# Kernel optimization log

Measured on AMD Instinct MI355X. Metric: run time of the kernel, lower is better.

The kernel has to match this reference:

```python
import jax, jax.numpy as jnp
import numpy as np

B, S, D = 4, 1024, 1024
L, H, DK, DV, DFF = 2, 8, 128, 128, 2048
MASK_VALUE = -1e-30
LN_EPS = 1e-14  # K.epsilon()**2 with K.epsilon()=1e-7


def _glorot(key, shape):
    fan_in, fan_out = shape[-2], shape[-1]
    lim = np.sqrt(6.0 / (fan_in + fan_out)).astype(np.float32)
    return jax.random.uniform(key, shape, jnp.float32, -lim, lim)


def setup_inputs() -> dict:
    key = jax.random.key(0)
    ks = jax.random.split(key, 8)
    return {
        "x": jax.random.normal(ks[0], (B, S, D), jnp.float32),
        "mask": jnp.ones((B, S), jnp.float32),
        "Wq": _glorot(ks[1], (L, H, D, DK)),
        "Wk": _glorot(ks[2], (L, H, D, DK)),
        "Wv": _glorot(ks[3], (L, H, D, DV)),
        "Wo": _glorot(ks[4], (L, H * DV, D)),
        "W1": _glorot(ks[5], (L, D, DFF)),
        "b1": jnp.zeros((L, DFF), jnp.float32),
        "W2": _glorot(ks[6], (L, DFF, D)),
        "b2": jnp.zeros((L, D), jnp.float32),
        "gamma": jnp.ones((2 * L,), jnp.float32),
        "beta": jnp.zeros((2 * L,), jnp.float32),
    }


def _layernorm(x, g, b):
    mean = jnp.mean(x, axis=-1, keepdims=True)
    var = jnp.mean(jnp.square(x - mean), axis=-1, keepdims=True)
    return (x - mean) / jnp.sqrt(var + LN_EPS) * g + b


def reference(x, mask, Wq, Wk, Wv, Wo, W1, b1, W2, b2, gamma, beta):
    m = mask[:, None, None, :]  # [B,1,1,S] broadcast over heads and query positions
    num_layers = Wq.shape[0]
    for i in range(num_layers):
        # All heads at once (faithful to the per-head loop: identical math)
        q = jnp.einsum("bsd,hdk->bhsk", x, Wq[i])
        k = jnp.einsum("bsd,hdk->bhsk", x, Wk[i])
        v = jnp.einsum("bsd,hdv->bhsv", x, Wv[i])
        A = jnp.einsum("bhsk,bhtk->bhst", q, k)  # NOTE: no 1/sqrt(dk) scaling in original
        A = m * A + (1.0 - m) * MASK_VALUE
        A = jax.nn.softmax(A, axis=-1)
        o = jnp.einsum("bhst,bhtv->bhsv", A, v)
        conc = o.transpose(0, 2, 1, 3).reshape(x.shape[0], x.shape[1], -1)  # [B,S,H*DV]
        proj = conc @ Wo[i]
        x = _layernorm(x + proj, gamma[2 * i], beta[2 * i])
        ffn = jax.nn.relu(x @ W1[i] + b1[i]) @ W2[i] + b2[i]
        x = _layernorm(x + ffn, gamma[2 * i + 1], beta[2 * i + 1])
    return x
```

## Files before the change

kernel.cpp:

```cpp
#include <hip/hip_runtime.h>
#include <hip/hip_bf16.h>


typedef __bf16 bf16_t;
typedef bf16_t bf16x8 __attribute__((ext_vector_type(8)));
typedef bf16_t bf16x4v __attribute__((ext_vector_type(4)));
typedef float f32x4 __attribute__((ext_vector_type(4)));

#define MFMA16(a, b, c) __builtin_amdgcn_mfma_f32_16x16x32_bf16((a), (b), (c), 0, 0, 0)

__device__ __align__(256) unsigned char g_ws[(size_t)192 << 20];

#define MBOFF(x) ((size_t)(x) << 20)
#define OFF_X32 MBOFF(0)
#define OFF_XB_HI MBOFF(16)
#define OFF_XB_LO MBOFF(24)
#define OFF_QKV_HI MBOFF(32)
#define OFF_QKV_LO MBOFF(56)
#define OFF_VT_HI MBOFF(80)
#define OFF_VT_LO MBOFF(88)
#define OFF_CONC_HI MBOFF(96)
#define OFF_CONC_LO MBOFF(104)
#define OFF_TMP MBOFF(112)
#define OFF_H_HI MBOFF(128)
#define OFF_H_LO MBOFF(144)
#define OFF_WQKV_HI MBOFF(160)
#define OFF_WQKV_LO MBOFF(166)
#define OFF_WO_HI MBOFF(172)
#define OFF_WO_LO MBOFF(174)
#define OFF_W1_HI MBOFF(176)
#define OFF_W1_LO MBOFF(180)
#define OFF_W2_HI MBOFF(184)
#define OFF_W2_LO MBOFF(188)

__device__ __forceinline__ void split2(float v, bf16_t& h, bf16_t& l) {
  h = (bf16_t)v;
  l = (bf16_t)(v - (float)h);
}

__device__ __forceinline__ void gl2lds16(const bf16_t* g, bf16_t* l) {
  __builtin_amdgcn_global_load_lds(
      (const __attribute__((address_space(1))) unsigned int*)(g),
      (__attribute__((address_space(3))) unsigned int*)(l), 16, 0, 0);
}

template <int EPI>
__global__ __launch_bounds__(512) void gemm_bt(
    size_t a_hi, size_t a_lo, size_t b_hi, size_t b_lo,
    size_t c0o, size_t c1o, const float* __restrict__ bias, int M, int N, int K) {
  const bf16_t* Ah = (const bf16_t*)(g_ws + a_hi);
  const bf16_t* Al = (const bf16_t*)(g_ws + a_lo);
  const bf16_t* Bh = (const bf16_t*)(g_ws + b_hi);
  const bf16_t* Bl = (const bf16_t*)(g_ws + b_lo);
  float* Cf = (float*)(g_ws + c0o);
  bf16_t* Ch = (bf16_t*)(g_ws + c0o);
  bf16_t* Cl = (bf16_t*)(g_ws + c1o);
  __shared__ __align__(16) bf16_t Ash[128 * 32];
  __shared__ __align__(16) bf16_t Asl[128 * 32];
  __shared__ __align__(16) bf16_t Bsh[128 * 32];
  __shared__ __align__(16) bf16_t Bsl[128 * 32];
  const int tid = threadIdx.x;
  const int wave = tid >> 6, lane = tid & 63;
  const int quad = lane >> 4, l16 = lane & 15;
  const int wm = wave & 3, wn = wave >> 2;
  const int m0 = blockIdx.y * 128, n0 = blockIdx.x * 128;
  const int srow = wave * 16 + (lane >> 2);
  const int scp = (lane & 3) ^ ((srow >> 1) & 3);
  const long agoff = (long)(m0 + srow) * K + scp * 8;
  const long bgoff = (long)(n0 + srow) * K + scp * 8;
  bf16_t* ldsA = Ash + wave * 512;
  bf16_t* ldsAl = Asl + wave * 512;
  bf16_t* ldsB = Bsh + wave * 512;
  bf16_t* ldsBl = Bsl + wave * 512;
  int aOff[2], bOff[4];
#pragma unroll
  for (int mt = 0; mt < 2; ++mt) {
    int R = wm * 32 + mt * 16 + l16;
    aOff[mt] = R * 32 + ((quad ^ ((R >> 1) & 3)) * 8);
  }
#pragma unroll
  for (int nt = 0; nt < 4; ++nt) {
    int R = wn * 64 + nt * 16 + l16;
    bOff[nt] = R * 32 + ((quad ^ ((R >> 1) & 3)) * 8);
  }
  f32x4 acc[2][4] = {};

  for (int k0 = 0; k0 < K; k0 += 32) {
    gl2lds16(Ah + agoff + k0, ldsA);
    gl2lds16(Al + agoff + k0, ldsAl);
    gl2lds16(Bh + bgoff + k0, ldsB);
    gl2lds16(Bl + bgoff + k0, ldsBl);
    __syncthreads();
    bf16x8 ah[2], al[2], bhf[4], blf[4];
#pragma unroll
    for (int mt = 0; mt < 2; ++mt) {
      ah[mt] = *(const bf16x8*)(Ash + aOff[mt]);
      al[mt] = *(const bf16x8*)(Asl + aOff[mt]);
    }
#pragma unroll
    for (int nt = 0; nt < 4; ++nt) {
      bhf[nt] = *(const bf16x8*)(Bsh + bOff[nt]);
      blf[nt] = *(const bf16x8*)(Bsl + bOff[nt]);
    }
#pragma unroll
    for (int mt = 0; mt < 2; ++mt)
#pragma unroll
      for (int nt = 0; nt < 4; ++nt) {
        acc[mt][nt] = MFMA16(ah[mt], bhf[nt], acc[mt][nt]);
        acc[mt][nt] = MFMA16(ah[mt], blf[nt], acc[mt][nt]);
        acc[mt][nt] = MFMA16(al[mt], bhf[nt], acc[mt][nt]);
      }
    __syncthreads();
  }

#pragma unroll
  for (int mt = 0; mt < 2; ++mt) {
    const int row0 = m0 + wm * 32 + mt * 16 + quad * 4;
#pragma unroll
    for (int nt = 0; nt < 4; ++nt) {
      const int col = n0 + wn * 64 + nt * 16 + l16;
      float bv = (EPI >= 2) ? bias[col] : 0.0f;
#pragma unroll
      for (int r = 0; r < 4; ++r) {
        float v = acc[mt][nt][r] + bv;
        if (EPI == 2) v = fmaxf(v, 0.0f);
        long off = (long)(row0 + r) * N + col;
        if (EPI == 0 || EPI == 3) {
          Cf[off] = v;
        } else {
          bf16_t h, l;
          split2(v, h, l);
          Ch[off] = h;
          Cl[off] = l;
        }
      }
    }
  }
}

__global__ __launch_bounds__(256) void attn_kernel(const float* __restrict__ mask) {
  const bf16_t* QKVh = (const bf16_t*)(g_ws + OFF_QKV_HI);
  const bf16_t* QKVl = (const bf16_t*)(g_ws + OFF_QKV_LO);
  const bf16_t* VTh = (const bf16_t*)(g_ws + OFF_VT_HI);
  const bf16_t* VTl = (const bf16_t*)(g_ws + OFF_VT_LO);
  bf16_t* conch = (bf16_t*)(g_ws + OFF_CONC_HI);
  bf16_t* concl = (bf16_t*)(g_ws + OFF_CONC_LO);
  __shared__ __align__(16) bf16_t Ksh[64 * 128];
  __shared__ __align__(16) bf16_t Ksl[64 * 128];
  __shared__ __align__(16) bf16_t Vsh[128 * 64];
  __shared__ __align__(16) bf16_t Vsl[128 * 64];
  __shared__ __align__(16) bf16_t Ps[4][16 * 72];
  const int tid = threadIdx.x;
  const int wave = tid >> 6, lane = tid & 63;
  const int quad = lane >> 4, l16 = lane & 15;
  const int q0 = blockIdx.x * 64;
  const int bh = blockIdx.y, b = bh >> 3, h = bh & 7;

  bf16x8 qfh[4], qfl[4];
  const long qgbase = ((long)(b * 1024) + q0 + wave * 16 + l16) * 3072 + h * 128;
#pragma unroll
  for (int ks = 0; ks < 4; ++ks) {
    qfh[ks] = *(const bf16x8*)(QKVh + qgbase + ks * 32 + quad * 8);
    qfl[ks] = *(const bf16x8*)(QKVl + qgbase + ks * 32 + quad * 8);
  }

  const int sKrow4 = wave * 16 + (lane >> 4);
  const int sVrow = wave * 32 + (lane >> 3);
  const int sVc = (lane & 7) ^ (sVrow & 7);
  const long vgbase = (long)bh * 131072 + (long)sVrow * 1024 + sVc * 8;

  f32x4 o[8] = {};
  float mi[4] = {-1e30f, -1e30f, -1e30f, -1e30f};
  float li[4] = {0.f, 0.f, 0.f, 0.f};

  for (int t0 = 0; t0 < 1024; t0 += 64) {
#pragma unroll
    for (int j = 0; j < 4; ++j) {
      const int r = sKrow4 + j * 4;
      const int c = (lane & 15) ^ ((r & 7) * 2);
      const long kg = ((long)(b * 1024) + t0 + r) * 3072 + 1024 + h * 128 + c * 8;
      gl2lds16(QKVh + kg, Ksh + (wave * 16 + j * 4) * 128);
      gl2lds16(QKVl + kg, Ksl + (wave * 16 + j * 4) * 128);
    }
#pragma unroll
    for (int j = 0; j < 4; ++j) {
      const long vg = vgbase + (long)(j * 8) * 1024 + t0;
      gl2lds16(VTh + vg, Vsh + (wave * 32 + j * 8) * 64);
      gl2lds16(VTl + vg, Vsl + (wave * 32 + j * 8) * 64);
    }
    __syncthreads();
    f32x4 s4[4] = {};
#pragma unroll
    for (int nt = 0; nt < 4; ++nt) {
      const int krow = nt * 16 + l16;
      const int ksw = (krow & 7) * 2;
#pragma unroll
      for (int ks = 0; ks < 4; ++ks) {
        const int so = krow * 128 + (((ks * 4 + quad) ^ ksw) * 8);
        bf16x8 kfh = *(const bf16x8*)(Ksh + so);
        bf16x8 kfl = *(const bf16x8*)(Ksl + so);
        s4[nt] = MFMA16(qfh[ks], kfh, s4[nt]);
        s4[nt] = MFMA16(qfh[ks], kfl, s4[nt]);
        s4[nt] = MFMA16(qfl[ks], kfh, s4[nt]);
      }
    }
#pragma unroll
    for (int nt = 0; nt < 4; ++nt) {
      float mv = mask[b * 1024 + t0 + nt * 16 + l16];
      float addv = (1.0f - mv) * (-1e-30f);
#pragma unroll
      for (int r = 0; r < 4; ++r) s4[nt][r] = mv * s4[nt][r] + addv;
    }
#pragma unroll
    for (int r = 0; r < 4; ++r) {
      float mx = fmaxf(fmaxf(s4[0][r], s4[1][r]), fmaxf(s4[2][r], s4[3][r]));
#pragma unroll
      for (int off = 1; off < 16; off <<= 1) mx = fmaxf(mx, __shfl_xor(mx, off, 64));
      float mnew = fmaxf(mi[r], mx);
      float alpha = __expf(mi[r] - mnew);
      float rs = 0.0f;
#pragma unroll
      for (int nt = 0; nt < 4; ++nt) {
        float p = __expf(s4[nt][r] - mnew);
        s4[nt][r] = p;
        rs += p;
      }
#pragma unroll
      for (int off = 1; off < 16; off <<= 1) rs += __shfl_xor(rs, off, 64);
      li[r] = li[r] * alpha + rs;
      mi[r] = mnew;
#pragma unroll
      for (int on = 0; on < 8; ++on) o[on][r] *= alpha;
    }
#pragma unroll
    for (int nt = 0; nt < 4; ++nt)
#pragma unroll
      for (int r = 0; r < 4; ++r)
        Ps[wave][(quad * 4 + r) * 72 + nt * 16 + l16] = (bf16_t)s4[nt][r];
    bf16x8 pf[2];
#pragma unroll
    for (int k2 = 0; k2 < 2; ++k2)
      pf[k2] = *(const bf16x8*)(&Ps[wave][l16 * 72 + k2 * 32 + quad * 8]);
#pragma unroll
    for (int k2 = 0; k2 < 2; ++k2) {
#pragma unroll
      for (int on = 0; on < 8; ++on) {
        const int vrow = on * 16 + l16;
        const int so = vrow * 64 + (((k2 * 4 + quad) ^ (vrow & 7)) * 8);
        bf16x8 vfh = *(const bf16x8*)(Vsh + so);
        bf16x8 vfl = *(const bf16x8*)(Vsl + so);
        o[on] = MFMA16(pf[k2], vfh, o[on]);
        o[on] = MFMA16(pf[k2], vfl, o[on]);
      }
    }
    __syncthreads();
  }
  const int srow_o = q0 + wave * 16 + quad * 4;
#pragma unroll
  for (int r = 0; r < 4; ++r) {
    float inv = 1.0f / li[r];
#pragma unroll
    for (int on = 0; on < 8; ++on) {
      float v = o[on][r] * inv;
      bf16_t hh, ll;
      split2(v, hh, ll);
      long off = (long)(b * 1024 + srow_o + r) * 1024 + h * 128 + on * 16 + l16;
      conch[off] = hh;
      concl[off] = ll;
    }
  }
}

__global__ __launch_bounds__(256) void ln_kernel(
    const float* __restrict__ gamma, const float* __restrict__ beta, int gidx,
    float* __restrict__ extf) {
  const float* xres = (const float*)(g_ws + OFF_X32);
  const float* y = (const float*)(g_ws + OFF_TMP);
  float* xout = (float*)(g_ws + OFF_X32);
  bf16_t* xbh = (bf16_t*)(g_ws + OFF_XB_HI);
  bf16_t* xbl = (bf16_t*)(g_ws + OFF_XB_LO);
  const int row = blockIdx.x, tid = threadIdx.x;
  const int wave = tid >> 6, lane = tid & 63;
  const long base = (long)row * 1024 + tid * 4;
  float4 xv = *(const float4*)(xres + base);
  float4 yv = *(const float4*)(y + base);
  float v0 = xv.x + yv.x, v1 = xv.y + yv.y, v2 = xv.z + yv.z, v3 = xv.w + yv.w;
  float s1 = v0 + v1 + v2 + v3;
  float s2 = v0 * v0 + v1 * v1 + v2 * v2 + v3 * v3;
#pragma unroll
  for (int off = 1; off < 64; off <<= 1) {
    s1 += __shfl_xor(s1, off, 64);
    s2 += __shfl_xor(s2, off, 64);
  }
  __shared__ __align__(16) float r1[4], r2[4];
  if (lane == 0) { r1[wave] = s1; r2[wave] = s2; }
  __syncthreads();
  s1 = r1[0] + r1[1] + r1[2] + r1[3];
  s2 = r2[0] + r2[1] + r2[2] + r2[3];
  const float mean = s1 * (1.0f / 1024.0f);
  float var = s2 * (1.0f / 1024.0f) - mean * mean;
  var = fmaxf(var, 0.0f);
  const float inv = rsqrtf(var + 1e-14f);
  const float g = gamma[gidx], be = beta[gidx];
  float o0 = (v0 - mean) * inv * g + be;
  float o1 = (v1 - mean) * inv * g + be;
  float o2 = (v2 - mean) * inv * g + be;
  float o3 = (v3 - mean) * inv * g + be;
  float4 ov = {o0, o1, o2, o3};
  *(float4*)(xout + base) = ov;
  if (extf) {
    *(float4*)(extf + base) = ov;
  } else {
    bf16_t h0, l0, h1, l1, h2, l2, h3, l3;
    split2(o0, h0, l0); split2(o1, h1, l1);
    split2(o2, h2, l2); split2(o3, h3, l3);
    bf16x4v hv = {h0, h1, h2, h3};
    bf16x4v lv = {l0, l1, l2, l3};
    *(bf16x4v*)(xbh + base) = hv;
    *(bf16x4v*)(xbl + base) = lv;
  }
}

__global__ __launch_bounds__(256) void cast_f2b(const float* __restrict__ in) {
  float* out = (float*)(g_ws + OFF_X32);
  bf16_t* outh = (bf16_t*)(g_ws + OFF_XB_HI);
  bf16_t* outl = (bf16_t*)(g_ws + OFF_XB_LO);
  long i = ((long)blockIdx.x * 256 + threadIdx.x) * 4;
  float4 v = *(const float4*)(in + i);
  *(float4*)(out + i) = v;
  bf16_t h0, l0, h1, l1, h2, l2, h3, l3;
  split2(v.x, h0, l0); split2(v.y, h1, l1);
  split2(v.z, h2, l2); split2(v.w, h3, l3);
  bf16x4v hv = {h0, h1, h2, h3};
  bf16x4v lv = {l0, l1, l2, l3};
  *(bf16x4v*)(outh + i) = hv;
  *(bf16x4v*)(outl + i) = lv;
}

__global__ __launch_bounds__(256) void transp_split(
    const float* __restrict__ in, size_t oh_off, size_t ol_off, int R, int C) {
  bf16_t* oh = (bf16_t*)(g_ws + oh_off);
  bf16_t* ol = (bf16_t*)(g_ws + ol_off);
  __shared__ float tile[32][33];
  const int tx = threadIdx.x, ty = threadIdx.y;
  const int c0 = blockIdx.x * 32, r0 = blockIdx.y * 32;
#pragma unroll
  for (int j = 0; j < 4; ++j)
    tile[ty + j * 8][tx] = in[(long)(r0 + ty + j * 8) * C + c0 + tx];
  __syncthreads();
#pragma unroll
  for (int j = 0; j < 4; ++j) {
    float v = tile[tx][ty + j * 8];
    bf16_t h, l;
    split2(v, h, l);
    long off = (long)(c0 + ty + j * 8) * R + r0 + tx;
    oh[off] = h;
    ol[off] = l;
  }
}

__global__ __launch_bounds__(256) void qkvw_trans(
    const float* __restrict__ Wq, const float* __restrict__ Wk,
    const float* __restrict__ Wv) {
  bf16_t* oh = (bf16_t*)(g_ws + OFF_WQKV_HI);
  bf16_t* ol = (bf16_t*)(g_ws + OFF_WQKV_LO);
  __shared__ float tile[32][33];
  const int tx = threadIdx.x, ty = threadIdx.y;
  const int z = blockIdx.z, mat = z >> 3, h = z & 7;
  const float* src = (mat == 0 ? Wq : (mat == 1 ? Wk : Wv)) + h * 131072;
  const int c0 = blockIdx.x * 32, r0 = blockIdx.y * 32;
#pragma unroll
  for (int j = 0; j < 4; ++j)
    tile[ty + j * 8][tx] = src[(r0 + ty + j * 8) * 128 + c0 + tx];
  __syncthreads();
  const int nbase = mat * 1024 + h * 128;
#pragma unroll
  for (int j = 0; j < 4; ++j) {
    float v = tile[tx][ty + j * 8];
    bf16_t hh, ll;
    split2(v, hh, ll);
    long off = (long)(nbase + c0 + ty + j * 8) * 1024 + r0 + tx;
    oh[off] = hh;
    ol[off] = ll;
  }
}

__global__ __launch_bounds__(256) void vt_trans() {
  const bf16_t* QKVh = (const bf16_t*)(g_ws + OFF_QKV_HI);
  const bf16_t* QKVl = (const bf16_t*)(g_ws + OFF_QKV_LO);
  bf16_t* VTh = (bf16_t*)(g_ws + OFF_VT_HI);
  bf16_t* VTl = (bf16_t*)(g_ws + OFF_VT_LO);
  __shared__ bf16_t th[32][34];
  __shared__ bf16_t tl[32][34];
  const int tx = threadIdx.x, ty = threadIdx.y;
  const int bh = blockIdx.z, b = bh >> 3, h = bh & 7;
  const int s0 = blockIdx.x * 32, v0 = blockIdx.y * 32;
#pragma unroll
  for (int j = 0; j < 4; ++j) {
    long src = ((long)(b * 1024) + s0 + ty + j * 8) * 3072 + 2048 + h * 128 + v0 + tx;
    th[ty + j * 8][tx] = QKVh[src];
    tl[ty + j * 8][tx] = QKVl[src];
  }
  __syncthreads();
#pragma unroll
  for (int j = 0; j < 4; ++j) {
    long off = (long)bh * 131072 + (long)(v0 + ty + j * 8) * 1024 + s0 + tx;
    VTh[off] = th[tx][ty + j * 8];
    VTl[off] = tl[tx][ty + j * 8];
  }
}

extern "C" void kernel_launch(void* const* d_in, const int* in_sizes, int n_in,
                              void* d_out, int out_size, void* d_ws, size_t ws_size,
                              hipStream_t stream) {
  const float* x_in = (const float*)d_in[0];
  const float* mask = (const float*)d_in[1];
  const float* Wq = (const float*)d_in[2];
  const float* Wk = (const float*)d_in[3];
  const float* Wv = (const float*)d_in[4];
  const float* Wo = (const float*)d_in[5];
  const float* W1 = (const float*)d_in[6];
  const float* b1 = (const float*)d_in[7];
  const float* W2 = (const float*)d_in[8];
  const float* b2 = (const float*)d_in[9];
  const float* gamma = (const float*)d_in[10];
  const float* beta = (const float*)d_in[11];
  float* out = (float*)d_out;
  (void)d_ws; (void)ws_size; (void)in_sizes; (void)n_in; (void)out_size;

  const dim3 tb(32, 8);
  cast_f2b<<<4096, 256, 0, stream>>>(x_in);

  for (int l = 0; l < 2; ++l) {
    qkvw_trans<<<dim3(4, 32, 24), tb, 0, stream>>>(
        Wq + (long)l * 1048576, Wk + (long)l * 1048576, Wv + (long)l * 1048576);
    transp_split<<<dim3(32, 32), tb, 0, stream>>>(Wo + (long)l * 1048576,
                                                  OFF_WO_HI, OFF_WO_LO, 1024, 1024);
    transp_split<<<dim3(64, 32), tb, 0, stream>>>(W1 + (long)l * 2097152,
                                                  OFF_W1_HI, OFF_W1_LO, 1024, 2048);
    transp_split<<<dim3(32, 64), tb, 0, stream>>>(W2 + (long)l * 2097152,
                                                  OFF_W2_HI, OFF_W2_LO, 2048, 1024);

    gemm_bt<1><<<dim3(24, 32), 512, 0, stream>>>(
        OFF_XB_HI, OFF_XB_LO, OFF_WQKV_HI, OFF_WQKV_LO,
        OFF_QKV_HI, OFF_QKV_LO, nullptr, 4096, 3072, 1024);
    vt_trans<<<dim3(32, 4, 32), tb, 0, stream>>>();
    attn_kernel<<<dim3(16, 32), 256, 0, stream>>>(mask);
    gemm_bt<0><<<dim3(8, 32), 512, 0, stream>>>(
        OFF_CONC_HI, OFF_CONC_LO, OFF_WO_HI, OFF_WO_LO,
        OFF_TMP, 0, nullptr, 4096, 1024, 1024);
    ln_kernel<<<4096, 256, 0, stream>>>(gamma, beta, 2 * l, nullptr);
    gemm_bt<2><<<dim3(16, 32), 512, 0, stream>>>(
        OFF_XB_HI, OFF_XB_LO, OFF_W1_HI, OFF_W1_LO,
        OFF_H_HI, OFF_H_LO, b1 + l * 2048, 4096, 2048, 1024);
    gemm_bt<3><<<dim3(8, 32), 512, 0, stream>>>(
        OFF_H_HI, OFF_H_LO, OFF_W2_HI, OFF_W2_LO,
        OFF_TMP, 0, b2 + l * 1024, 4096, 1024, 2048);
    ln_kernel<<<4096, 256, 0, stream>>>(gamma, beta, 2 * l + 1,
                                        (l == 1) ? out : nullptr);
  }
}
```

Baseline: 886.0 us.

## Rewrite GEMM with 128x256 tiles, double-buffered LDS pipeline, and split-K

```diff
diff --git a/kernel.cpp b/kernel.cpp
--- a/kernel.cpp
+++ b/kernel.cpp
@@ -32,6 +32,7 @@
 #define OFF_W1_LO MBOFF(180)
 #define OFF_W2_HI MBOFF(184)
 #define OFF_W2_LO MBOFF(188)
+#define OFF_TMP2 MBOFF(32)
 
 __device__ __forceinline__ void split2(float v, bf16_t& h, bf16_t& l) {
   h = (bf16_t)v;
@@ -45,81 +46,133 @@
 }
 
 template <int EPI>
-__global__ __launch_bounds__(512) void gemm_bt(
+__global__ __launch_bounds__(512, 2) void gemm8(
     size_t a_hi, size_t a_lo, size_t b_hi, size_t b_lo,
-    size_t c0o, size_t c1o, const float* __restrict__ bias, int M, int N, int K) {
+    size_t c0o, size_t c1o, const float* __restrict__ bias,
+    int M, int N, int Ktot, int Ksl) {
   const bf16_t* Ah = (const bf16_t*)(g_ws + a_hi);
   const bf16_t* Al = (const bf16_t*)(g_ws + a_lo);
   const bf16_t* Bh = (const bf16_t*)(g_ws + b_hi);
   const bf16_t* Bl = (const bf16_t*)(g_ws + b_lo);
-  float* Cf = (float*)(g_ws + c0o);
-  bf16_t* Ch = (bf16_t*)(g_ws + c0o);
-  bf16_t* Cl = (bf16_t*)(g_ws + c1o);
-  __shared__ __align__(16) bf16_t Ash[128 * 32];
-  __shared__ __align__(16) bf16_t Asl[128 * 32];
-  __shared__ __align__(16) bf16_t Bsh[128 * 32];
-  __shared__ __align__(16) bf16_t Bsl[128 * 32];
+  __shared__ __align__(16) bf16_t sAh[2][128 * 32];
+  __shared__ __align__(16) bf16_t sAl[2][128 * 32];
+  __shared__ __align__(16) bf16_t sBh[2][256 * 32];
+  __shared__ __align__(16) bf16_t sBl[2][256 * 32];
   const int tid = threadIdx.x;
   const int wave = tid >> 6, lane = tid & 63;
   const int quad = lane >> 4, l16 = lane & 15;
-  const int wm = wave & 3, wn = wave >> 2;
-  const int m0 = blockIdx.y * 128, n0 = blockIdx.x * 128;
+  const int wm = wave & 1, wn = wave >> 1;
+  const int m0 = blockIdx.y * 128, n0 = blockIdx.x * 256;
+  const int z = blockIdx.z;
+  const int kbase = z * Ksl;
+
   const int srow = wave * 16 + (lane >> 2);
   const int scp = (lane & 3) ^ ((srow >> 1) & 3);
-  const long agoff = (long)(m0 + srow) * K + scp * 8;
-  const long bgoff = (long)(n0 + srow) * K + scp * 8;
-  bf16_t* ldsA = Ash + wave * 512;
-  bf16_t* ldsAl = Asl + wave * 512;
-  bf16_t* ldsB = Bsh + wave * 512;
-  bf16_t* ldsBl = Bsl + wave * 512;
-  int aOff[2], bOff[4];
-#pragma unroll
-  for (int mt = 0; mt < 2; ++mt) {
-    int R = wm * 32 + mt * 16 + l16;
-    aOff[mt] = R * 32 + ((quad ^ ((R >> 1) & 3)) * 8);
-  }
-#pragma unroll
-  for (int nt = 0; nt < 4; ++nt) {
-    int R = wn * 64 + nt * 16 + l16;
-    bOff[nt] = R * 32 + ((quad ^ ((R >> 1) & 3)) * 8);
-  }
-  f32x4 acc[2][4] = {};
-
-  for (int k0 = 0; k0 < K; k0 += 32) {
-    gl2lds16(Ah + agoff + k0, ldsA);
-    gl2lds16(Al + agoff + k0, ldsAl);
-    gl2lds16(Bh + bgoff + k0, ldsB);
-    gl2lds16(Bl + bgoff + k0, ldsBl);
-    __syncthreads();
-    bf16x8 ah[2], al[2], bhf[4], blf[4];
+  const bf16_t* agh = Ah + (long)(m0 + srow) * Ktot + kbase + scp * 8;
+  const bf16_t* agl = Al + (long)(m0 + srow) * Ktot + kbase + scp * 8;
+  const bf16_t* bgh = Bh + (long)(n0 + srow) * Ktot + kbase + scp * 8;
+  const bf16_t* bgl = Bl + (long)(n0 + srow) * Ktot + kbase + scp * 8;
+  const long bstep = (long)128 * Ktot;
+
+  const int fsw = quad ^ ((l16 >> 1) & 3);
+  int aOff[4], bOff[4];
+#pragma unroll
+  for (int mt = 0; mt < 4; ++mt)
+    aOff[mt] = (wm * 64 + mt * 16 + l16) * 32 + fsw * 8;
+#pragma unroll
+  for (int nt = 0; nt < 4; ++nt)
+    bOff[nt] = (wn * 64 + nt * 16 + l16) * 32 + fsw * 8;
+
+  f32x4 acc[4][4] = {};
+  const int nk = Ksl >> 5;
+
+#define STAGE_PH1(bufi, ko)                            \
+  gl2lds16(agh + (ko), &sAh[bufi][wave * 512]);        \
+  gl2lds16(agl + (ko), &sAl[bufi][wave * 512]);        \
+  gl2lds16(bgh + (ko), &sBh[bufi][wave * 512]);
+#define STAGE_PH2(bufi, ko)                                      \
+  gl2lds16(bgh + bstep + (ko), &sBh[bufi][4096 + wave * 512]);   \
+  gl2lds16(bgl + (ko), &sBl[bufi][wave * 512]);                  \
+  gl2lds16(bgl + bstep + (ko), &sBl[bufi][4096 + wave * 512]);
+
+  STAGE_PH1(0, 0);
+  STAGE_PH2(0, 0);
+
+  for (int t = 0; t < nk; ++t) {
+    const int cur = t & 1, nxt = cur ^ 1;
+    const int ko = (t + 1) * 32;
+    const bool pf = (t + 1 < nk);
+    if (pf) {
+      STAGE_PH1(nxt, ko);
+      asm volatile("s_waitcnt vmcnt(3)" ::: "memory");
+    } else {
+      asm volatile("s_waitcnt vmcnt(0)" ::: "memory");
+    }
+    __builtin_amdgcn_sched_barrier(0);
+    __builtin_amdgcn_s_barrier();
+    __builtin_amdgcn_sched_barrier(0);
+    bf16x8 bh4[4], bl4[4], ah2[2], al2[2];
+#pragma unroll
+    for (int nt = 0; nt < 4; ++nt) {
+      bh4[nt] = *(const bf16x8*)(&sBh[cur][bOff[nt]]);
+      bl4[nt] = *(const bf16x8*)(&sBl[cur][bOff[nt]]);
+    }
 #pragma unroll
     for (int mt = 0; mt < 2; ++mt) {
-      ah[mt] = *(const bf16x8*)(Ash + aOff[mt]);
-      al[mt] = *(const bf16x8*)(Asl + aOff[mt]);
-    }
-#pragma unroll
-    for (int nt = 0; nt < 4; ++nt) {
-      bhf[nt] = *(const bf16x8*)(Bsh + bOff[nt]);
-      blf[nt] = *(const bf16x8*)(Bsl + bOff[nt]);
-    }
+      ah2[mt] = *(const bf16x8*)(&sAh[cur][aOff[mt]]);
+      al2[mt] = *(const bf16x8*)(&sAl[cur][aOff[mt]]);
+    }
+    asm volatile("s_waitcnt lgkmcnt(0)" ::: "memory");
+    __builtin_amdgcn_sched_barrier(0);
+    __builtin_amdgcn_s_setprio(1);
 #pragma unroll
     for (int mt = 0; mt < 2; ++mt)
 #pragma unroll
       for (int nt = 0; nt < 4; ++nt) {
-        acc[mt][nt] = MFMA16(ah[mt], bhf[nt], acc[mt][nt]);
-        acc[mt][nt] = MFMA16(ah[mt], blf[nt], acc[mt][nt]);
-        acc[mt][nt] = MFMA16(al[mt], bhf[nt], acc[mt][nt]);
+        acc[mt][nt] = MFMA16(ah2[mt], bh4[nt], acc[mt][nt]);
+        acc[mt][nt] = MFMA16(ah2[mt], bl4[nt], acc[mt][nt]);
+        acc[mt][nt] = MFMA16(al2[mt], bh4[nt], acc[mt][nt]);
       }
-    __syncthreads();
-  }
-
-#pragma unroll
-  for (int mt = 0; mt < 2; ++mt) {
-    const int row0 = m0 + wm * 32 + mt * 16 + quad * 4;
+    __builtin_amdgcn_s_setprio(0);
+    __builtin_amdgcn_sched_barrier(0);
+    __builtin_amdgcn_s_barrier();
+    if (pf) {
+      STAGE_PH2(nxt, ko);
+    }
+    bf16x8 ah2b[2], al2b[2];
+#pragma unroll
+    for (int mt = 0; mt < 2; ++mt) {
+      ah2b[mt] = *(const bf16x8*)(&sAh[cur][aOff[mt + 2]]);
+      al2b[mt] = *(const bf16x8*)(&sAl[cur][aOff[mt + 2]]);
+    }
+    asm volatile("s_waitcnt lgkmcnt(0)" ::: "memory");
+    __builtin_amdgcn_sched_barrier(0);
+    __builtin_amdgcn_s_setprio(1);
+#pragma unroll
+    for (int mt = 0; mt < 2; ++mt)
+#pragma unroll
+      for (int nt = 0; nt < 4; ++nt) {
+        acc[mt + 2][nt] = MFMA16(ah2b[mt], bh4[nt], acc[mt + 2][nt]);
+        acc[mt + 2][nt] = MFMA16(ah2b[mt], bl4[nt], acc[mt + 2][nt]);
+        acc[mt + 2][nt] = MFMA16(al2b[mt], bh4[nt], acc[mt + 2][nt]);
+      }
+    __builtin_amdgcn_s_setprio(0);
+    __builtin_amdgcn_sched_barrier(0);
+    __builtin_amdgcn_s_barrier();
+  }
+#undef STAGE_PH1
+#undef STAGE_PH2
+
+  float* Cf = (float*)(g_ws + (z == 0 ? c0o : c1o));
+  bf16_t* Ch = (bf16_t*)(g_ws + c0o);
+  bf16_t* Cl = (bf16_t*)(g_ws + c1o);
+#pragma unroll
+  for (int mt = 0; mt < 4; ++mt) {
+    const int row0 = m0 + wm * 64 + mt * 16 + quad * 4;
 #pragma unroll
     for (int nt = 0; nt < 4; ++nt) {
       const int col = n0 + wn * 64 + nt * 16 + l16;
-      float bv = (EPI >= 2) ? bias[col] : 0.0f;
+      float bv = ((EPI == 2 || EPI == 3) && z == 0) ? bias[col] : 0.0f;
 #pragma unroll
       for (int r = 0; r < 4; ++r) {
         float v = acc[mt][nt][r] + bv;
@@ -275,7 +328,8 @@
     const float* __restrict__ gamma, const float* __restrict__ beta, int gidx,
     float* __restrict__ extf) {
   const float* xres = (const float*)(g_ws + OFF_X32);
-  const float* y = (const float*)(g_ws + OFF_TMP);
+  const float* y1 = (const float*)(g_ws + OFF_TMP);
+  const float* y2 = (const float*)(g_ws + OFF_TMP2);
   float* xout = (float*)(g_ws + OFF_X32);
   bf16_t* xbh = (bf16_t*)(g_ws + OFF_XB_HI);
   bf16_t* xbl = (bf16_t*)(g_ws + OFF_XB_LO);
@@ -283,8 +337,10 @@
   const int wave = tid >> 6, lane = tid & 63;
   const long base = (long)row * 1024 + tid * 4;
   float4 xv = *(const float4*)(xres + base);
-  float4 yv = *(const float4*)(y + base);
-  float v0 = xv.x + yv.x, v1 = xv.y + yv.y, v2 = xv.z + yv.z, v3 = xv.w + yv.w;
+  float4 yv = *(const float4*)(y1 + base);
+  float4 y2v = *(const float4*)(y2 + base);
+  float v0 = xv.x + yv.x + y2v.x, v1 = xv.y + yv.y + y2v.y;
+  float v2 = xv.z + yv.z + y2v.z, v3 = xv.w + yv.w + y2v.w;
   float s1 = v0 + v1 + v2 + v3;
   float s2 = v0 * v0 + v1 * v1 + v2 * v2 + v3 * v3;
 #pragma unroll
@@ -441,21 +497,21 @@
     transp_split<<<dim3(32, 64), tb, 0, stream>>>(W2 + (long)l * 2097152,
                                                   OFF_W2_HI, OFF_W2_LO, 2048, 1024);
 
-    gemm_bt<1><<<dim3(24, 32), 512, 0, stream>>>(
+    gemm8<1><<<dim3(12, 32, 1), 512, 0, stream>>>(
         OFF_XB_HI, OFF_XB_LO, OFF_WQKV_HI, OFF_WQKV_LO,
-        OFF_QKV_HI, OFF_QKV_LO, nullptr, 4096, 3072, 1024);
+        OFF_QKV_HI, OFF_QKV_LO, nullptr, 4096, 3072, 1024, 1024);
     vt_trans<<<dim3(32, 4, 32), tb, 0, stream>>>();
     attn_kernel<<<dim3(16, 32), 256, 0, stream>>>(mask);
-    gemm_bt<0><<<dim3(8, 32), 512, 0, stream>>>(
+    gemm8<0><<<dim3(4, 32, 2), 512, 0, stream>>>(
         OFF_CONC_HI, OFF_CONC_LO, OFF_WO_HI, OFF_WO_LO,
-        OFF_TMP, 0, nullptr, 4096, 1024, 1024);
+        OFF_TMP, OFF_TMP2, nullptr, 4096, 1024, 1024, 512);
     ln_kernel<<<4096, 256, 0, stream>>>(gamma, beta, 2 * l, nullptr);
-    gemm_bt<2><<<dim3(16, 32), 512, 0, stream>>>(
+    gemm8<2><<<dim3(8, 32, 1), 512, 0, stream>>>(
         OFF_XB_HI, OFF_XB_LO, OFF_W1_HI, OFF_W1_LO,
-        OFF_H_HI, OFF_H_LO, b1 + l * 2048, 4096, 2048, 1024);
-    gemm_bt<3><<<dim3(8, 32), 512, 0, stream>>>(
+        OFF_H_HI, OFF_H_LO, b1 + l * 2048, 4096, 2048, 1024, 1024);
+    gemm8<3><<<dim3(4, 32, 2), 512, 0, stream>>>(
         OFF_H_HI, OFF_H_LO, OFF_W2_HI, OFF_W2_LO,
-        OFF_TMP, 0, b2 + l * 1024, 4096, 1024, 2048);
+        OFF_TMP, OFF_TMP2, b2 + l * 1024, 4096, 1024, 2048, 1024);
     ln_kernel<<<4096, 256, 0, stream>>>(gamma, beta, 2 * l + 1,
                                         (l == 1) ? out : nullptr);
   }
```

New measurement: 873.2 us. Within noise of the previous version (-1.4%).

## Split-K the N=1024 output GEMMs in two and sum partials in layernorm

Applied to the files above, without the earlier changes.

```diff
diff --git a/kernel.cpp b/kernel.cpp
--- a/kernel.cpp
+++ b/kernel.cpp
@@ -32,6 +32,7 @@
 #define OFF_W1_LO MBOFF(180)
 #define OFF_W2_HI MBOFF(184)
 #define OFF_W2_LO MBOFF(188)
+#define OFF_TMP2 MBOFF(32)
 
 __device__ __forceinline__ void split2(float v, bf16_t& h, bf16_t& l) {
   h = (bf16_t)v;
@@ -47,14 +48,12 @@
 template <int EPI>
 __global__ __launch_bounds__(512) void gemm_bt(
     size_t a_hi, size_t a_lo, size_t b_hi, size_t b_lo,
-    size_t c0o, size_t c1o, const float* __restrict__ bias, int M, int N, int K) {
+    size_t c0o, size_t c1o, const float* __restrict__ bias,
+    int M, int N, int Ktot, int Ksl) {
   const bf16_t* Ah = (const bf16_t*)(g_ws + a_hi);
   const bf16_t* Al = (const bf16_t*)(g_ws + a_lo);
   const bf16_t* Bh = (const bf16_t*)(g_ws + b_hi);
   const bf16_t* Bl = (const bf16_t*)(g_ws + b_lo);
-  float* Cf = (float*)(g_ws + c0o);
-  bf16_t* Ch = (bf16_t*)(g_ws + c0o);
-  bf16_t* Cl = (bf16_t*)(g_ws + c1o);
   __shared__ __align__(16) bf16_t Ash[128 * 32];
   __shared__ __align__(16) bf16_t Asl[128 * 32];
   __shared__ __align__(16) bf16_t Bsh[128 * 32];
@@ -64,10 +63,11 @@
   const int quad = lane >> 4, l16 = lane & 15;
   const int wm = wave & 3, wn = wave >> 2;
   const int m0 = blockIdx.y * 128, n0 = blockIdx.x * 128;
+  const int z = blockIdx.z;
   const int srow = wave * 16 + (lane >> 2);
   const int scp = (lane & 3) ^ ((srow >> 1) & 3);
-  const long agoff = (long)(m0 + srow) * K + scp * 8;
-  const long bgoff = (long)(n0 + srow) * K + scp * 8;
+  const long agoff = (long)(m0 + srow) * Ktot + (long)z * Ksl + scp * 8;
+  const long bgoff = (long)(n0 + srow) * Ktot + (long)z * Ksl + scp * 8;
   bf16_t* ldsA = Ash + wave * 512;
   bf16_t* ldsAl = Asl + wave * 512;
   bf16_t* ldsB = Bsh + wave * 512;
@@ -85,7 +85,7 @@
   }
   f32x4 acc[2][4] = {};
 
-  for (int k0 = 0; k0 < K; k0 += 32) {
+  for (int k0 = 0; k0 < Ksl; k0 += 32) {
     gl2lds16(Ah + agoff + k0, ldsA);
     gl2lds16(Al + agoff + k0, ldsAl);
     gl2lds16(Bh + bgoff + k0, ldsB);
@@ -113,13 +113,16 @@
     __syncthreads();
   }
 
+  float* Cf = (float*)(g_ws + (z == 0 ? c0o : c1o));
+  bf16_t* Ch = (bf16_t*)(g_ws + c0o);
+  bf16_t* Cl = (bf16_t*)(g_ws + c1o);
 #pragma unroll
   for (int mt = 0; mt < 2; ++mt) {
     const int row0 = m0 + wm * 32 + mt * 16 + quad * 4;
 #pragma unroll
     for (int nt = 0; nt < 4; ++nt) {
       const int col = n0 + wn * 64 + nt * 16 + l16;
-      float bv = (EPI >= 2) ? bias[col] : 0.0f;
+      float bv = ((EPI >= 2) && z == 0) ? bias[col] : 0.0f;
 #pragma unroll
       for (int r = 0; r < 4; ++r) {
         float v = acc[mt][nt][r] + bv;
@@ -275,7 +278,8 @@
     const float* __restrict__ gamma, const float* __restrict__ beta, int gidx,
     float* __restrict__ extf) {
   const float* xres = (const float*)(g_ws + OFF_X32);
-  const float* y = (const float*)(g_ws + OFF_TMP);
+  const float* y1 = (const float*)(g_ws + OFF_TMP);
+  const float* y2 = (const float*)(g_ws + OFF_TMP2);
   float* xout = (float*)(g_ws + OFF_X32);
   bf16_t* xbh = (bf16_t*)(g_ws + OFF_XB_HI);
   bf16_t* xbl = (bf16_t*)(g_ws + OFF_XB_LO);
@@ -283,8 +287,10 @@
   const int wave = tid >> 6, lane = tid & 63;
   const long base = (long)row * 1024 + tid * 4;
   float4 xv = *(const float4*)(xres + base);
-  float4 yv = *(const float4*)(y + base);
-  float v0 = xv.x + yv.x, v1 = xv.y + yv.y, v2 = xv.z + yv.z, v3 = xv.w + yv.w;
+  float4 yv = *(const float4*)(y1 + base);
+  float4 y2v = *(const float4*)(y2 + base);
+  float v0 = xv.x + yv.x + y2v.x, v1 = xv.y + yv.y + y2v.y;
+  float v2 = xv.z + yv.z + y2v.z, v3 = xv.w + yv.w + y2v.w;
   float s1 = v0 + v1 + v2 + v3;
   float s2 = v0 * v0 + v1 * v1 + v2 * v2 + v3 * v3;
 #pragma unroll
@@ -441,21 +447,21 @@
     transp_split<<<dim3(32, 64), tb, 0, stream>>>(W2 + (long)l * 2097152,
                                                   OFF_W2_HI, OFF_W2_LO, 2048, 1024);
 
-    gemm_bt<1><<<dim3(24, 32), 512, 0, stream>>>(
+    gemm_bt<1><<<dim3(24, 32, 1), 512, 0, stream>>>(
         OFF_XB_HI, OFF_XB_LO, OFF_WQKV_HI, OFF_WQKV_LO,
-        OFF_QKV_HI, OFF_QKV_LO, nullptr, 4096, 3072, 1024);
+        OFF_QKV_HI, OFF_QKV_LO, nullptr, 4096, 3072, 1024, 1024);
     vt_trans<<<dim3(32, 4, 32), tb, 0, stream>>>();
     attn_kernel<<<dim3(16, 32), 256, 0, stream>>>(mask);
-    gemm_bt<0><<<dim3(8, 32), 512, 0, stream>>>(
+    gemm_bt<0><<<dim3(8, 32, 2), 512, 0, stream>>>(
         OFF_CONC_HI, OFF_CONC_LO, OFF_WO_HI, OFF_WO_LO,
-        OFF_TMP, 0, nullptr, 4096, 1024, 1024);
+        OFF_TMP, OFF_TMP2, nullptr, 4096, 1024, 1024, 512);
     ln_kernel<<<4096, 256, 0, stream>>>(gamma, beta, 2 * l, nullptr);
-    gemm_bt<2><<<dim3(16, 32), 512, 0, stream>>>(
+    gemm_bt<2><<<dim3(16, 32, 1), 512, 0, stream>>>(
         OFF_XB_HI, OFF_XB_LO, OFF_W1_HI, OFF_W1_LO,
-        OFF_H_HI, OFF_H_LO, b1 + l * 2048, 4096, 2048, 1024);
-    gemm_bt<3><<<dim3(8, 32), 512, 0, stream>>>(
+        OFF_H_HI, OFF_H_LO, b1 + l * 2048, 4096, 2048, 1024, 1024);
+    gemm_bt<3><<<dim3(8, 32, 2), 512, 0, stream>>>(
         OFF_H_HI, OFF_H_LO, OFF_W2_HI, OFF_W2_LO,
-        OFF_TMP, 0, b2 + l * 1024, 4096, 1024, 2048);
+        OFF_TMP, OFF_TMP2, b2 + l * 1024, 4096, 1024, 2048, 1024);
     ln_kernel<<<4096, 256, 0, stream>>>(gamma, beta, 2 * l + 1,
                                         (l == 1) ? out : nullptr);
   }
```

After: 835.1 us. 1.06x faster.
